# Performance work log

Measured on AMD Instinct MI355X. Metric: run time of the kernel, lower is better.

## Reference

```python
import jax, jax.numpy as jnp
import numpy as np

HARD_NUM = 700      # hardcoded self.hard_num in HardOIMLoss
OIM_SCALAR = 30.0   # oim_scalar init arg
N, D, P, Q = 4096, 256, 5532, 5000


def _l2norm(x):
    return x / jnp.linalg.norm(x, axis=-1, keepdims=True)


def setup_inputs() -> dict:
    key = jax.random.key(0)
    k1, k2, k3, k4, k5 = jax.random.split(key, 5)
    # OIM features and lookup tables are L2-normalized rows
    inputs = _l2norm(jax.random.normal(k1, (N, D), dtype=jnp.float32))
    lut = _l2norm(jax.random.normal(k2, (P, D), dtype=jnp.float32))
    cq = _l2norm(jax.random.normal(k3, (Q, D), dtype=jnp.float32))
    reliability = jax.random.uniform(k4, (P + Q,), dtype=jnp.float32)
    labels = jax.random.randint(k5, (N,), 0, P, dtype=jnp.int32)
    return {"inputs": inputs, "labels": labels, "lut": lut, "cq": cq,
            "reliability": reliability}


def reference(inputs, labels, lut, cq, reliability):
    # projected[n, c] = <inputs_n, table_c> * reliability_c ;  table = [lut; cq]
    table = jnp.concatenate([lut, cq], axis=0)            # [P+Q, D]
    projected = (inputs @ table.T) * reliability[None, :]  # [N, P+Q]
    C = projected.shape[1]
    # value at sorted-descending index HARD_NUM == (HARD_NUM+1)-th largest
    boundary = jax.lax.top_k(projected, HARD_NUM + 1)[0][:, -1]  # [N]
    hard_mask = projected >= boundary[:, None]
    label_mask = jnp.arange(C, dtype=labels.dtype)[None, :] == labels[:, None]
    mask = hard_mask | label_mask
    logits = jnp.where(mask, projected * OIM_SCALAR, -jnp.inf)
    # cross entropy (mean over rows); label column is always unmasked
    logZ = jax.scipy.special.logsumexp(logits, axis=1)
    tgt = jnp.take_along_axis(logits, labels[:, None].astype(jnp.int32), axis=1)[:, 0]
    return jnp.mean(logZ - tgt)
```

## Files before the change

### kernel.cpp

```cpp
#include <hip/hip_runtime.h>
#include <math.h>

#define N_ROWS 4096
#define DIM    256
#define P_SZ   5532
#define Q_SZ   5000
#define C_COLS 10532
#define TPAD   10624
#define PSTR   10624
#define NGR    (PSTR / 8)
#define K_SEL  701
#define SCALAR 30.0f
#define C2     (SCALAR * 1.4426950408889634f)

typedef __attribute__((ext_vector_type(8))) short   short8;
typedef __attribute__((ext_vector_type(4))) float   float4_t;
typedef __attribute__((ext_vector_type(4))) unsigned short ushort4_t;
typedef __attribute__((ext_vector_type(8))) unsigned short ushort8_t;

__device__ __forceinline__ unsigned short f2bf(float f) {
    unsigned u = __float_as_uint(f);
    unsigned r = u + 0x7FFFu + ((u >> 16) & 1u);
    return (unsigned short)(r >> 16);
}
__device__ __forceinline__ float bf2f(unsigned short u) {
    return __uint_as_float((unsigned)u << 16);
}
__device__ __forceinline__ unsigned short key16(unsigned short u) {
    return (u & 0x8000u) ? (unsigned short)(~u) : (unsigned short)(u | 0x8000u);
}
__device__ __forceinline__ float key2f16(unsigned key) {
    unsigned short b = (key & 0x8000u) ? (unsigned short)(key & 0x7FFFu)
                                       : (unsigned short)(~key & 0xFFFFu);
    return bf2f(b);
}
__device__ __forceinline__ void gload16(const void* g, void* l) {
    __builtin_amdgcn_global_load_lds(
        (const __attribute__((address_space(1))) unsigned int*)g,
        (__attribute__((address_space(3))) unsigned int*)l, 16, 0, 0);
}

#define NIN_G  (N_ROWS * DIM / 4)
#define NTAB_G (TPAD * DIM / 4)

__global__ __launch_bounds__(256) void convert_bf16(
    const float* __restrict__ inputs, const float* __restrict__ lut,
    const float* __restrict__ cq, unsigned short* __restrict__ in_bf,
    unsigned short* __restrict__ tab_bf)
{
    const int g = blockIdx.x * 256 + threadIdx.x;
    if (g >= NIN_G + NTAB_G) return;
    float4_t v;
    unsigned short* dst;
    if (g < NIN_G) {
        v = *(const float4_t*)&inputs[(size_t)g * 4];
        dst = in_bf + (size_t)g * 4;
    } else {
        const int t = g - NIN_G;
        const int row = t >> 6;
        const int c4  = (t & 63) * 4;
        if (row < P_SZ)        v = *(const float4_t*)&lut[(size_t)row * DIM + c4];
        else if (row < C_COLS) v = *(const float4_t*)&cq[(size_t)(row - P_SZ) * DIM + c4];
        else                   v = (float4_t){0.f, 0.f, 0.f, 0.f};
        dst = tab_bf + (size_t)t * 4;
    }
    ushort4_t h = { f2bf(v.x), f2bf(v.y), f2bf(v.z), f2bf(v.w) };
    *(ushort4_t*)dst = h;
}

#define NWG_X 83
#define NWG_Y 32
#define NWG   (NWG_X * NWG_Y)
#define CSTR  132

__global__ __launch_bounds__(256) void gemm_proj(
    const unsigned short* __restrict__ in_bf,
    const unsigned short* __restrict__ tab_bf,
    const float* __restrict__ rel,
    unsigned short* __restrict__ proj)
{
    __shared__ __align__(16) unsigned short smem[128 * CSTR];
    unsigned short* At = smem;
    unsigned short* Bt = smem + 128 * 64;

    const int tid  = threadIdx.x;
    const int lane = tid & 63, wid = tid >> 6;
    const int wm = wid >> 1, wn = wid & 1;

    const int phys = blockIdx.x;
    const int wg   = (phys & 7) * (NWG / 8) + (phys >> 3);
    const int bx   = wg >> 5;
    const int by   = wg & 31;
    const int row0 = by * 128, col0 = bx * 128;

    float4_t acc[4][4];
    #pragma unroll
    for (int i = 0; i < 4; ++i)
        #pragma unroll
        for (int j = 0; j < 4; ++j)
            acc[i][j] = (float4_t){0.f, 0.f, 0.f, 0.f};

    for (int k0 = 0; k0 < DIM; k0 += 64) {
        #pragma unroll
        for (int it = 0; it < 4; ++it) {
            const int g  = it * 256 + tid;
            const int r  = g >> 3;
            const int kb = ((g & 7) * 16) ^ ((r & 7) << 4);
            gload16(in_bf  + (size_t)(row0 + r) * DIM + k0 + (kb >> 1),
                    (char*)At + g * 16);
            gload16(tab_bf + (size_t)(col0 + r) * DIM + k0 + (kb >> 1),
                    (char*)Bt + g * 16);
        }
        __syncthreads();

        #pragma unroll
        for (int kk = 0; kk < 2; ++kk) {
            const int krow = lane & 15;
            const int kb   = kk * 64 + ((lane >> 4) << 4);
            short8 af[4], bfr[4];
            #pragma unroll
            for (int i = 0; i < 4; ++i) {
                const int r = wm * 64 + i * 16 + krow;
                af[i] = *(const short8*)((const char*)At + (r * 128 + (kb ^ ((r & 7) << 4))));
            }
            #pragma unroll
            for (int j = 0; j < 4; ++j) {
                const int r = wn * 64 + j * 16 + krow;
                bfr[j] = *(const short8*)((const char*)Bt + (r * 128 + (kb ^ ((r & 7) << 4))));
            }
            #pragma unroll
            for (int i = 0; i < 4; ++i)
                #pragma unroll
                for (int j = 0; j < 4; ++j)
                    acc[i][j] = __builtin_amdgcn_mfma_f32_16x16x32_bf16(af[i], bfr[j], acc[i][j], 0, 0, 0);
        }
        __syncthreads();
    }

    const int lr = (lane >> 4) << 2;
    const int lc = lane & 15;
    #pragma unroll
    for (int j = 0; j < 4; ++j) {
        const int cl  = wn * 64 + j * 16 + lc;
        const int col = col0 + cl;
        const bool pad = (col >= C_COLS);
        const float rl = pad ? 0.f : rel[col];
        #pragma unroll
        for (int i = 0; i < 4; ++i) {
            const int rbase = wm * 64 + i * 16 + lr;
            #pragma unroll
            for (int rr = 0; rr < 4; ++rr)
                smem[(rbase + rr) * CSTR + cl] =
                    pad ? (unsigned short)0u : key16(f2bf(acc[i][j][rr] * rl));
        }
    }
    __syncthreads();
    #pragma unroll
    for (int it = 0; it < 8; ++it) {
        const int g = it * 256 + tid;
        const int r = g >> 4;
        const int c8 = (g & 15) * 8;
        *(ushort8_t*)(proj + (size_t)(row0 + r) * PSTR + col0 + c8) =
            *(const ushort8_t*)&smem[r * CSTR + c8];
    }
}

__global__ __launch_bounds__(256) void row_loss_kernel(
    const unsigned short* __restrict__ proj, const int* __restrict__ labels,
    float* __restrict__ row_loss)
{
    __shared__ unsigned hist[2][2048];
    __shared__ unsigned h2[32];
    __shared__ float    e2[32];
    __shared__ unsigned wsum[4];
    __shared__ float    fsum[4];
    __shared__ unsigned sel_bin, sel_k, sel_sub;
    __shared__ float    sel_minor;

    const int tid = threadIdx.x, lane = tid & 63, wid = tid >> 6;
    const int hsel = wid >> 1;
    const int row = blockIdx.x;
    const ushort8_t* prow = (const ushort8_t*)(proj + (size_t)row * PSTR);

    for (int i = tid; i < 4096; i += 256) hist[0][i] = 0;
    if (tid < 32) { h2[tid] = 0; e2[tid] = 0.f; }
    __syncthreads();

    ushort8_t r[6];
    #pragma unroll
    for (int it = 0; it < 6; ++it) {
        const int g = it * 256 + tid;
        if (it < 5 || g < NGR) {
            r[it] = prow[g];
            #pragma unroll
            for (int e = 0; e < 8; ++e)
                atomicAdd(&hist[hsel][r[it][e] >> 5], 1u);
        }
    }
    __syncthreads();

    {
        const int t8 = tid * 8;
        unsigned cnt[8];
        unsigned s = 0;
        #pragma unroll
        for (int b = 0; b < 8; ++b) {
            cnt[b] = hist[0][t8 + b] + hist[1][t8 + b];
            s += cnt[b];
        }
        unsigned incl = s;
        #pragma unroll
        for (int off = 1; off < 64; off <<= 1) {
            const unsigned t = __shfl_down(incl, off, 64);
            if (lane + off < 64) incl += t;
        }
        if (lane == 0) wsum[wid] = incl;
        __syncthreads();
        unsigned cum = incl - s;
        for (int w = wid + 1; w < 4; ++w) cum += wsum[w];
        #pragma unroll
        for (int b = 7; b >= 0; --b) {
            const unsigned c = cnt[b];
            if (cum < K_SEL && cum + c >= K_SEL) {
                sel_bin = (unsigned)(t8 + b); sel_k = K_SEL - cum;
            }
            cum += c;
        }
    }
    __syncthreads();
    const unsigned b1 = sel_bin;
    const unsigned k2 = sel_k;
    const unsigned klo = b1 << 5, khi = (b1 + 1) << 5;

    float above = 0.f;
    #pragma unroll
    for (int it = 0; it < 6; ++it) {
        const int g = it * 256 + tid;
        if (it < 5 || g < NGR) {
            #pragma unroll
            for (int e = 0; e < 8; ++e) {
                const unsigned key = r[it][e];
                if (key >= khi) {
                    above += exp2f(C2 * (key2f16(key) - 1.0f));
                } else if (key >= klo) {
                    atomicAdd(&h2[key & 31u], 1u);
                    atomicAdd(&e2[key & 31u], exp2f(C2 * (key2f16(key) - 1.0f)));
                }
            }
        }
    }
    #pragma unroll
    for (int off = 1; off < 64; off <<= 1) {
        const float t = __shfl_down(above, off, 64);
        if (lane + off < 64) above += t;
    }
    if (lane == 0) fsum[wid] = above;
    __syncthreads();

    if (wid == 0) {
        const unsigned c = (lane < 32) ? h2[lane] : 0u;
        const float    f = (lane < 32) ? e2[lane] : 0.f;
        unsigned ic = c; float fc = f;
        #pragma unroll
        for (int off = 1; off < 64; off <<= 1) {
            const unsigned tc = __shfl_down(ic, off, 64);
            const float    tf = __shfl_down(fc, off, 64);
            if (lane + off < 64) { ic += tc; fc += tf; }
        }
        const unsigned abv = ic - c;
        if (lane < 32 && abv < k2 && abv + c >= k2) {
            sel_sub = (unsigned)lane; sel_minor = fc;
        }
    }
    __syncthreads();

    if (tid == 0) {
        const unsigned bkey = (b1 << 5) | sel_sub;
        float total = fsum[0] + fsum[1] + fsum[2] + fsum[3] + sel_minor;
        const unsigned ulk = ((const unsigned short*)prow)[labels[row]];
        const float pl = key2f16(ulk);
        if (ulk < bkey) total += exp2f(C2 * (pl - 1.0f));
        row_loss[row] = SCALAR * 1.0f + logf(total) - SCALAR * pl;
    }
}

__global__ __launch_bounds__(256) void final_reduce(
    const float* __restrict__ row_loss, float* __restrict__ out)
{
    __shared__ float fred[4];
    const int tid = threadIdx.x, lane = tid & 63, wid = tid >> 6;
    float s = 0.f;
    for (int i = tid; i < N_ROWS; i += 256) s += row_loss[i];
    #pragma unroll
    for (int off = 1; off < 64; off <<= 1) {
        const float t = __shfl_down(s, off, 64);
        if (lane + off < 64) s += t;
    }
    if (lane == 0) fred[wid] = s;
    __syncthreads();
    if (tid == 0) out[0] = (fred[0] + fred[1] + fred[2] + fred[3]) / (float)N_ROWS;
}

extern "C" void kernel_launch(void* const* d_in, const int* in_sizes, int n_in,
                              void* d_out, int out_size, void* d_ws, size_t ws_size,
                              hipStream_t stream) {
    const float* inputs = (const float*)d_in[0];
    const int*   labels = (const int*)d_in[1];
    const float* lut    = (const float*)d_in[2];
    const float* cq     = (const float*)d_in[3];
    const float* rel    = (const float*)d_in[4];
    float* out = (float*)d_out;

    unsigned short* in_bf  = (unsigned short*)d_ws;
    unsigned short* tab_bf = in_bf  + (size_t)N_ROWS * DIM;
    unsigned short* proj   = tab_bf + (size_t)TPAD * DIM;
    float* rl_buf = (float*)(proj + (size_t)N_ROWS * PSTR);

    convert_bf16<<<(NIN_G + NTAB_G) / 256, 256, 0, stream>>>(inputs, lut, cq, in_bf, tab_bf);
    gemm_proj<<<NWG, 256, 0, stream>>>(in_bf, tab_bf, rel, proj);
    row_loss_kernel<<<N_ROWS, 256, 0, stream>>>(proj, labels, rl_buf);
    final_reduce<<<1, 256, 0, stream>>>(rl_buf, out);
}
```

Measured before the change: 103.5 us.

## Use 8-bit radix select with replicated histograms and reread row from cache

Replaces the 11-bit/5-bit two-level histogram select with an 8-bit/8-bit radix select. The first-level histogram is spread across 16 padded replicas to cut LDS atomic contention. Rows are no longer held in registers; each of the three passes (histogram, sub-histogram, exp-sum) rereads the row from global/L2, and exp work is done only in the final pass. This trades extra memory reads for fewer register-resident values, less atomic contention and simpler selection logic.

Result: faster. 97.59 us (-5.7%).

```diff
diff --git a/kernel.cpp b/kernel.cpp
--- a/kernel.cpp
+++ b/kernel.cpp
@@ -9,6 +9,7 @@
 #define TPAD   10624
 #define PSTR   10624
 #define NGR    (PSTR / 8)
+#define NDW    (PSTR / 4)
 #define K_SEL  701
 #define SCALAR 30.0f
 #define C2     (SCALAR * 1.4426950408889634f)
@@ -17,6 +18,7 @@
 typedef __attribute__((ext_vector_type(4))) float   float4_t;
 typedef __attribute__((ext_vector_type(4))) unsigned short ushort4_t;
 typedef __attribute__((ext_vector_type(8))) unsigned short ushort8_t;
+typedef __attribute__((ext_vector_type(4))) unsigned int  uint4_t;
 
 __device__ __forceinline__ unsigned short f2bf(float f) {
     unsigned u = __float_as_uint(f);
@@ -165,50 +167,50 @@
     }
 }
 
+#define NCPY 16
 __global__ __launch_bounds__(256) void row_loss_kernel(
     const unsigned short* __restrict__ proj, const int* __restrict__ labels,
     float* __restrict__ row_loss)
 {
-    __shared__ unsigned hist[2][2048];
-    __shared__ unsigned h2[32];
-    __shared__ float    e2[32];
+    __shared__ unsigned h1[NCPY * 257];
+    __shared__ unsigned h2[256];
     __shared__ unsigned wsum[4];
     __shared__ float    fsum[4];
     __shared__ unsigned sel_bin, sel_k, sel_sub;
-    __shared__ float    sel_minor;
 
     const int tid = threadIdx.x, lane = tid & 63, wid = tid >> 6;
-    const int hsel = wid >> 1;
     const int row = blockIdx.x;
-    const ushort8_t* prow = (const ushort8_t*)(proj + (size_t)row * PSTR);
-
-    for (int i = tid; i < 4096; i += 256) hist[0][i] = 0;
-    if (tid < 32) { h2[tid] = 0; e2[tid] = 0.f; }
-    __syncthreads();
-
-    ushort8_t r[6];
-    #pragma unroll
-    for (int it = 0; it < 6; ++it) {
-        const int g = it * 256 + tid;
-        if (it < 5 || g < NGR) {
-            r[it] = prow[g];
-            #pragma unroll
-            for (int e = 0; e < 8; ++e)
-                atomicAdd(&hist[hsel][r[it][e] >> 5], 1u);
+    const uint4_t* prow = (const uint4_t*)(proj + (size_t)row * PSTR);
+    const unsigned cbase = (unsigned)(tid & (NCPY - 1)) * 257;
+
+    for (int i = tid; i < NCPY * 257; i += 256) h1[i] = 0;
+    if (tid < 256) h2[tid] = 0;
+    __syncthreads();
+
+    #pragma unroll
+    for (int it = 0; it < 5; ++it) {
+        const uint4_t w = prow[it * 256 + tid];
+        #pragma unroll
+        for (int d = 0; d < 4; ++d) {
+            atomicAdd(&h1[cbase + ((w[d] >> 8) & 0xFFu)], 1u);
+            atomicAdd(&h1[cbase + (w[d] >> 24)], 1u);
+        }
+    }
+    if (tid < NGR - 1280) {
+        const uint4_t w = prow[1280 + tid];
+        #pragma unroll
+        for (int d = 0; d < 4; ++d) {
+            atomicAdd(&h1[cbase + ((w[d] >> 8) & 0xFFu)], 1u);
+            atomicAdd(&h1[cbase + (w[d] >> 24)], 1u);
         }
     }
     __syncthreads();
 
     {
-        const int t8 = tid * 8;
-        unsigned cnt[8];
-        unsigned s = 0;
-        #pragma unroll
-        for (int b = 0; b < 8; ++b) {
-            cnt[b] = hist[0][t8 + b] + hist[1][t8 + b];
-            s += cnt[b];
-        }
-        unsigned incl = s;
+        unsigned c = 0;
+        #pragma unroll
+        for (int cp = 0; cp < NCPY; ++cp) c += h1[cp * 257 + tid];
+        unsigned incl = c;
         #pragma unroll
         for (int off = 1; off < 64; off <<= 1) {
             const unsigned t = __shfl_down(incl, off, 64);
@@ -216,70 +218,88 @@
         }
         if (lane == 0) wsum[wid] = incl;
         __syncthreads();
-        unsigned cum = incl - s;
-        for (int w = wid + 1; w < 4; ++w) cum += wsum[w];
-        #pragma unroll
-        for (int b = 7; b >= 0; --b) {
-            const unsigned c = cnt[b];
-            if (cum < K_SEL && cum + c >= K_SEL) {
-                sel_bin = (unsigned)(t8 + b); sel_k = K_SEL - cum;
-            }
-            cum += c;
+        unsigned above = incl - c;
+        for (int w = wid + 1; w < 4; ++w) above += wsum[w];
+        if (above < K_SEL && above + c >= K_SEL) {
+            sel_bin = (unsigned)tid; sel_k = K_SEL - above;
         }
     }
     __syncthreads();
     const unsigned b1 = sel_bin;
     const unsigned k2 = sel_k;
-    const unsigned klo = b1 << 5, khi = (b1 + 1) << 5;
-
-    float above = 0.f;
-    #pragma unroll
-    for (int it = 0; it < 6; ++it) {
-        const int g = it * 256 + tid;
-        if (it < 5 || g < NGR) {
-            #pragma unroll
-            for (int e = 0; e < 8; ++e) {
-                const unsigned key = r[it][e];
-                if (key >= khi) {
-                    above += exp2f(C2 * (key2f16(key) - 1.0f));
-                } else if (key >= klo) {
-                    atomicAdd(&h2[key & 31u], 1u);
-                    atomicAdd(&e2[key & 31u], exp2f(C2 * (key2f16(key) - 1.0f)));
-                }
-            }
+    __syncthreads();
+
+    #pragma unroll
+    for (int it = 0; it < 5; ++it) {
+        const uint4_t w = prow[it * 256 + tid];
+        #pragma unroll
+        for (int d = 0; d < 4; ++d) {
+            const unsigned lo = w[d] & 0xFFFFu, hi = w[d] >> 16;
+            if ((lo >> 8) == b1) atomicAdd(&h2[lo & 0xFFu], 1u);
+            if ((hi >> 8) == b1) atomicAdd(&h2[hi & 0xFFu], 1u);
+        }
+    }
+    if (tid < NGR - 1280) {
+        const uint4_t w = prow[1280 + tid];
+        #pragma unroll
+        for (int d = 0; d < 4; ++d) {
+            const unsigned lo = w[d] & 0xFFFFu, hi = w[d] >> 16;
+            if ((lo >> 8) == b1) atomicAdd(&h2[lo & 0xFFu], 1u);
+            if ((hi >> 8) == b1) atomicAdd(&h2[hi & 0xFFu], 1u);
+        }
+    }
+    __syncthreads();
+
+    {
+        const unsigned c = h2[tid];
+        unsigned incl = c;
+        #pragma unroll
+        for (int off = 1; off < 64; off <<= 1) {
+            const unsigned t = __shfl_down(incl, off, 64);
+            if (lane + off < 64) incl += t;
+        }
+        if (lane == 0) wsum[wid] = incl;
+        __syncthreads();
+        unsigned above = incl - c;
+        for (int w = wid + 1; w < 4; ++w) above += wsum[w];
+        if (above < k2 && above + c >= k2) sel_sub = (unsigned)tid;
+    }
+    __syncthreads();
+    const unsigned bkey = (b1 << 8) | sel_sub;
+
+    float s = 0.f;
+    #pragma unroll
+    for (int it = 0; it < 5; ++it) {
+        const uint4_t w = prow[it * 256 + tid];
+        #pragma unroll
+        for (int d = 0; d < 4; ++d) {
+            const unsigned lo = w[d] & 0xFFFFu, hi = w[d] >> 16;
+            if (lo >= bkey) s += exp2f(C2 * key2f16(lo) - C2);
+            if (hi >= bkey) s += exp2f(C2 * key2f16(hi) - C2);
+        }
+    }
+    if (tid < NGR - 1280) {
+        const uint4_t w = prow[1280 + tid];
+        #pragma unroll
+        for (int d = 0; d < 4; ++d) {
+            const unsigned lo = w[d] & 0xFFFFu, hi = w[d] >> 16;
+            if (lo >= bkey) s += exp2f(C2 * key2f16(lo) - C2);
+            if (hi >= bkey) s += exp2f(C2 * key2f16(hi) - C2);
         }
     }
     #pragma unroll
     for (int off = 1; off < 64; off <<= 1) {
-        const float t = __shfl_down(above, off, 64);
-        if (lane + off < 64) above += t;
-    }
-    if (lane == 0) fsum[wid] = above;
-    __syncthreads();
-
-    if (wid == 0) {
-        const unsigned c = (lane < 32) ? h2[lane] : 0u;
-        const float    f = (lane < 32) ? e2[lane] : 0.f;
-        unsigned ic = c; float fc = f;
-        #pragma unroll
-        for (int off = 1; off < 64; off <<= 1) {
-            const unsigned tc = __shfl_down(ic, off, 64);
-            const float    tf = __shfl_down(fc, off, 64);
-            if (lane + off < 64) { ic += tc; fc += tf; }
-        }
-        const unsigned abv = ic - c;
-        if (lane < 32 && abv < k2 && abv + c >= k2) {
-            sel_sub = (unsigned)lane; sel_minor = fc;
-        }
-    }
+        const float t = __shfl_down(s, off, 64);
+        if (lane + off < 64) s += t;
+    }
+    if (lane == 0) fsum[wid] = s;
     __syncthreads();
 
     if (tid == 0) {
-        const unsigned bkey = (b1 << 5) | sel_sub;
-        float total = fsum[0] + fsum[1] + fsum[2] + fsum[3] + sel_minor;
+        float total = fsum[0] + fsum[1] + fsum[2] + fsum[3];
         const unsigned ulk = ((const unsigned short*)prow)[labels[row]];
         const float pl = key2f16(ulk);
-        if (ulk < bkey) total += exp2f(C2 * (pl - 1.0f));
+        if (ulk < bkey) total += exp2f(C2 * pl - C2);
         row_loss[row] = SCALAR * 1.0f + logf(total) - SCALAR * pl;
     }
 }
```
